# Optimization experiments

Measured on AMD Instinct MI355X. Metric: run time of the kernel, lower is better.

The kernel has to match this reference:

```python
import jax, jax.numpy as jnp
import numpy as np

D_MODEL = 1024
N_HEADS = 16
SEQ = 2048
BATCH = 2
EPS = 1e-5


def layer_norm(x, g, b):
    mu = jnp.mean(x, axis=-1, keepdims=True)
    var = jnp.mean(jnp.square(x - mu), axis=-1, keepdims=True)
    return (x - mu) * jax.lax.rsqrt(var + EPS) * g + b


def setup_inputs() -> dict:
    key = jax.random.key(0)
    ks = jax.random.split(key, 10)
    D = D_MODEL
    s = lambda fan_in: 1.0 / np.sqrt(fan_in)
    return {
        "x": jax.random.normal(ks[0], (BATCH, SEQ, D), dtype=jnp.float32),
        # weights stored [in, out] (torch Linear is y = x @ W.T; equivalent math)
        "w_attn": jax.random.uniform(ks[1], (D, 3 * D), minval=-s(D), maxval=s(D), dtype=jnp.float32),
        "b_attn": jnp.zeros((3 * D,), jnp.float32),
        "w_proj": jax.random.uniform(ks[2], (D, D), minval=-s(D), maxval=s(D), dtype=jnp.float32),
        "b_proj": jnp.zeros((D,), jnp.float32),
        "ln1_g": jnp.ones((D,), jnp.float32),
        "ln1_b": jnp.zeros((D,), jnp.float32),
        "ln2_g": jnp.ones((D,), jnp.float32),
        "ln2_b": jnp.zeros((D,), jnp.float32),
        "w_fc1": jax.random.uniform(ks[3], (D, 4 * D), minval=-s(D), maxval=s(D), dtype=jnp.float32),
        "b_fc1": jnp.zeros((4 * D,), jnp.float32),
        "w_fc2": jax.random.uniform(ks[4], (4 * D, D), minval=-s(4 * D), maxval=s(4 * D), dtype=jnp.float32),
        "b_fc2": jnp.zeros((D,), jnp.float32),
    }


def reference(x, w_attn, b_attn, w_proj, b_proj, ln1_g, ln1_b, ln2_g, ln2_b, w_fc1, b_fc1, w_fc2, b_fc2):
    B, L, D = x.shape
    H = N_HEADS
    Dh = D // H

    # --- attention sublayer ---
    h = layer_norm(x, ln1_g, ln1_b)
    qkv = h @ w_attn + b_attn                      # [B, L, 3D]
    # SOURCE BUG (faithful): q, k, v are all taken from the k third.
    k = qkv[..., D:2 * D]
    kh = k.reshape(B, L, H, Dh).transpose(0, 2, 1, 3)   # [B, H, L, Dh]
    att = jnp.einsum('bhqd,bhkd->bhqk', kh, kh) / jnp.sqrt(jnp.float32(Dh))
    att = jax.nn.softmax(att, axis=-1)
    out = jnp.einsum('bhqk,bhkd->bhqd', att, kh)         # [B, H, L, Dh]
    out = out.transpose(0, 2, 1, 3).reshape(B, L, D)
    x = x + (out @ w_proj + b_proj)

    # --- feed-forward sublayer ---
    h = layer_norm(x, ln2_g, ln2_b)
    h = jax.nn.relu(h @ w_fc1 + b_fc1)
    x = x + (h @ w_fc2 + b_fc2)
    return x
```

## Files before the change

### kernel.cpp

```cpp
#include <hip/hip_runtime.h>


typedef __attribute__((ext_vector_type(8))) short s8v;
typedef __attribute__((ext_vector_type(4))) float f4v;

#define D_MODEL 1024
#define SEQ 2048
#define BATCH 2
#define NH 16
#define DH 64
#define MROWS (BATCH * SEQ)

__device__ __forceinline__ float b2f(unsigned short u) {
  union { unsigned int i; float f; } v; v.i = ((unsigned int)u) << 16; return v.f;
}
__device__ __forceinline__ unsigned short f2b(float f) {
  unsigned int i = __builtin_bit_cast(unsigned int, f);
  unsigned int r = (i + 0x7fffu + ((i >> 16) & 1u)) >> 16;
  return (unsigned short)r;
}
__device__ __forceinline__ void async16(const void* g, void* l) {
  __builtin_amdgcn_global_load_lds(
      (const __attribute__((address_space(1))) unsigned int*)g,
      (__attribute__((address_space(3))) unsigned int*)l, 16, 0, 0);
}
__device__ __forceinline__ unsigned short cvt_b(float f) { return f2b(f); }
__device__ __forceinline__ unsigned short cvt_b(unsigned short u) { return u; }

__global__ __launch_bounds__(256) void ln_kernel(
    const float* __restrict__ x, const float* __restrict__ g,
    const float* __restrict__ bb, unsigned short* __restrict__ out) {
  int row = blockIdx.x;
  int t = threadIdx.x;
  const float* xr = x + (size_t)row * D_MODEL;
  float v[4];
  float s = 0.f, s2 = 0.f;
#pragma unroll
  for (int i = 0; i < 4; ++i) {
    float f = xr[t + 256 * i];
    v[i] = f; s += f; s2 += f * f;
  }
#pragma unroll
  for (int off = 1; off < 64; off <<= 1) {
    s += __shfl_xor(s, off, 64);
    s2 += __shfl_xor(s2, off, 64);
  }
  __shared__ float red[8];
  if ((t & 63) == 0) { red[t >> 6] = s; red[4 + (t >> 6)] = s2; }
  __syncthreads();
  s = red[0] + red[1] + red[2] + red[3];
  s2 = red[4] + red[5] + red[6] + red[7];
  float mu = s * (1.f / D_MODEL);
  float var = s2 * (1.f / D_MODEL) - mu * mu;
  float rstd = rsqrtf(var + 1e-5f);
#pragma unroll
  for (int i = 0; i < 4; ++i) {
    int c = t + 256 * i;
    float h = (v[i] - mu) * rstd * g[c] + bb[c];
    out[(size_t)row * D_MODEL + c] = f2b(h);
  }
}

template <typename T>
__global__ __launch_bounds__(256) void transpose_b(
    const T* __restrict__ src, unsigned short* __restrict__ dst,
    int srcStride, int dstStride, long long srcBatch, long long dstBatch) {
  __shared__ unsigned short tile[64][65];
  const T* s = src + (size_t)blockIdx.z * srcBatch;
  unsigned short* d = dst + (size_t)blockIdx.z * dstBatch;
  int n0 = blockIdx.x * 64, k0 = blockIdx.y * 64;
  for (int i = threadIdx.x; i < 4096; i += 256) {
    int k = i >> 6, n = i & 63;
    tile[k][n] = cvt_b(s[(size_t)(k0 + k) * srcStride + n0 + n]);
  }
  __syncthreads();
  for (int i = threadIdx.x; i < 4096; i += 256) {
    int n = i >> 6, k = i & 63;
    d[(size_t)(n0 + n) * dstStride + k0 + k] = tile[k][n];
  }
}

template <int RES, bool RELU, bool KH, int OUTF, int BN>
__global__ __launch_bounds__(256) void gemm_bt(
    const unsigned short* __restrict__ A, const unsigned short* __restrict__ Bt,
    const float* __restrict__ bias, const float* __restrict__ res,
    void* __restrict__ out, int M, int N, int K) {
  constexpr int NT = BN / 32;
  __shared__ __align__(16) unsigned short lsA[128 * 64];
  __shared__ __align__(16) unsigned short lsB[BN * 64];
  int tid = threadIdx.x;
  int lane = tid & 63, w = tid >> 6, quad = lane >> 4, l16 = lane & 15;
  int m0 = blockIdx.y * 128, n0 = blockIdx.x * BN;
  int wm = (w >> 1) * 64, wn = (w & 1) * (BN / 2);
  f4v acc[4][NT] = {};
  for (int kt = 0; kt < K; kt += 64) {
#pragma unroll
    for (int i = 0; i < 4; ++i) {
      int cb = w * 256 + i * 64;
      int ci = cb + lane;
      int row = ci >> 3, c = ci & 7;
      int cs = c ^ (row & 7);
      async16(A + (size_t)(m0 + row) * K + kt + cs * 8, &lsA[cb * 8]);
    }
#pragma unroll
    for (int i = 0; i < BN / 32; ++i) {
      int cb = w * (BN * 2) + i * 64;
      int ci = cb + lane;
      int row = ci >> 3, c = ci & 7;
      int cs = c ^ (row & 7);
      async16(Bt + (size_t)(n0 + row) * K + kt + cs * 8, &lsB[cb * 8]);
    }
    __builtin_amdgcn_s_waitcnt(0x0f70);
    __syncthreads();
#pragma unroll
    for (int s = 0; s < 2; ++s) {
      s8v af[4], bf[NT];
#pragma unroll
      for (int t = 0; t < 4; ++t) {
        int am = wm + t * 16 + l16;
        int ac = (s * 4 + quad) ^ (am & 7);
        af[t] = *(const s8v*)(&lsA[am * 64 + ac * 8]);
      }
#pragma unroll
      for (int t = 0; t < NT; ++t) {
        int bn = wn + t * 16 + l16;
        int bc = (s * 4 + quad) ^ (bn & 7);
        bf[t] = *(const s8v*)(&lsB[bn * 64 + bc * 8]);
      }
#pragma unroll
      for (int ti = 0; ti < 4; ++ti)
#pragma unroll
        for (int tj = 0; tj < NT; ++tj)
          acc[ti][tj] = __builtin_amdgcn_mfma_f32_16x16x32_bf16(
              af[ti], bf[tj], acc[ti][tj], 0, 0, 0);
    }
    __syncthreads();
  }
#pragma unroll
  for (int tj = 0; tj < NT; ++tj) {
    int col = n0 + wn + tj * 16 + l16;
    float bv = bias[col];
#pragma unroll
    for (int ti = 0; ti < 4; ++ti) {
#pragma unroll
      for (int r = 0; r < 4; ++r) {
        int rowg = m0 + wm + ti * 16 + quad * 4 + r;
        float vv = acc[ti][tj][r] + bv;
        if (RES == 2) vv += res[(size_t)rowg * N + col];
        if (RELU) vv = fmaxf(vv, 0.f);
        size_t oidx;
        if (KH) {
          int b = rowg >> 11, l = rowg & 2047, h = col >> 6, d = col & 63;
          oidx = (((size_t)(b * NH + h)) * SEQ + l) * DH + d;
        } else {
          oidx = (size_t)rowg * N + col;
        }
        if (OUTF == 0) ((unsigned short*)out)[oidx] = f2b(vv);
        else           ((float*)out)[oidx] = vv;
      }
    }
  }
}

__global__ __launch_bounds__(256) void flash_k(
    const unsigned short* __restrict__ kh, const unsigned short* __restrict__ khT,
    float* __restrict__ Opart, float* __restrict__ lpart) {
  __shared__ __align__(16) unsigned short lsK[64 * 64];
  __shared__ __align__(16) unsigned short lsKT[64 * 64];
  __shared__ __align__(16) unsigned short lsP[4][32 * 72];
  int tid = threadIdx.x;
  int lane = tid & 63, w = tid >> 6, quad = lane >> 4, l16 = lane & 15;
  int qb = blockIdx.x, bh = blockIdx.y, split = blockIdx.z;
  const unsigned short* khB = kh + (size_t)bh * SEQ * DH;
  const unsigned short* khTB = khT + (size_t)bh * DH * SEQ;
  float* Op = Opart + (size_t)split * MROWS * D_MODEL;
  float* lp = lpart + (size_t)split * BATCH * NH * SEQ;
  s8v aQ[2][2];
#pragma unroll
  for (int g = 0; g < 2; ++g) {
    int q = qb * 128 + w * 32 + g * 16 + l16;
#pragma unroll
    for (int s = 0; s < 2; ++s)
      aQ[g][s] = *(const s8v*)(khB + (size_t)q * DH + s * 32 + quad * 8);
  }
  float l_part[2][4] = {};
  f4v accO[2][4] = {};
  const float kexp = 0.18033688f;

  for (int kt = split * 16; kt < split * 16 + 16; ++kt) {
#pragma unroll
    for (int i = 0; i < 2; ++i) {
      int cb = w * 128 + i * 64;
      int ci = cb + lane;
      int row = ci >> 3, c = ci & 7;
      int cs = c ^ (row & 7);
      async16(khB + (size_t)(kt * 64 + row) * DH + cs * 8, &lsK[cb * 8]);
      async16(khTB + (size_t)row * SEQ + kt * 64 + cs * 8, &lsKT[cb * 8]);
    }
    __builtin_amdgcn_s_waitcnt(0x0f70);
    __syncthreads();
    f4v accS[2][4] = {};
#pragma unroll
    for (int s = 0; s < 2; ++s) {
#pragma unroll
      for (int tj = 0; tj < 4; ++tj) {
        int key = tj * 16 + l16;
        int c = (s * 4 + quad) ^ (key & 7);
        s8v bK = *(const s8v*)(&lsK[key * 64 + c * 8]);
#pragma unroll
        for (int g = 0; g < 2; ++g)
          accS[g][tj] = __builtin_amdgcn_mfma_f32_16x16x32_bf16(
              aQ[g][s], bK, accS[g][tj], 0, 0, 0);
      }
    }
    unsigned short* Pb = lsP[w];
#pragma unroll
    for (int g = 0; g < 2; ++g)
#pragma unroll
      for (int tj = 0; tj < 4; ++tj)
#pragma unroll
        for (int r = 0; r < 4; ++r) {
          float p = exp2f(accS[g][tj][r] * kexp);
          l_part[g][r] += p;
          unsigned int pb = __builtin_bit_cast(unsigned int, p * 1.00195312f);
          Pb[(g * 16 + quad * 4 + r) * 72 + tj * 16 + l16] =
              (unsigned short)(pb >> 16);
        }
#pragma unroll
    for (int s2 = 0; s2 < 2; ++s2) {
      s8v aP[2];
#pragma unroll
      for (int g = 0; g < 2; ++g)
        aP[g] = *(const s8v*)(&Pb[(g * 16 + l16) * 72 + s2 * 32 + quad * 8]);
#pragma unroll
      for (int db = 0; db < 4; ++db) {
        int d = db * 16 + l16;
        int c = (s2 * 4 + quad) ^ (d & 7);
        s8v bV = *(const s8v*)(&lsKT[d * 64 + c * 8]);
#pragma unroll
        for (int g = 0; g < 2; ++g)
          accO[g][db] = __builtin_amdgcn_mfma_f32_16x16x32_bf16(
              aP[g], bV, accO[g][db], 0, 0, 0);
      }
    }
    __syncthreads();
  }
  int b = bh >> 4, h = bh & 15;
#pragma unroll
  for (int g = 0; g < 2; ++g)
#pragma unroll
    for (int r = 0; r < 4; ++r) {
      float lpv = l_part[g][r];
#pragma unroll
      for (int off = 1; off < 16; off <<= 1) lpv += __shfl_xor(lpv, off, 64);
      int l = qb * 128 + w * 32 + g * 16 + quad * 4 + r;
      if (l16 == 0) lp[(size_t)bh * SEQ + l] = lpv;
#pragma unroll
      for (int db = 0; db < 4; ++db) {
        int d = db * 16 + l16;
        Op[((size_t)(b * SEQ + l)) * D_MODEL + h * DH + d] = accO[g][db][r];
      }
    }
}

__global__ __launch_bounds__(256) void attn_combine(
    const float* __restrict__ Opart, const float* __restrict__ lpart,
    unsigned short* __restrict__ attn) {
  int row = blockIdx.x;
  int b = row >> 11, l = row & 2047;
  int c0 = threadIdx.x * 4;
  int h = c0 >> 6;
  size_t lidx = (size_t)(b * NH + h) * SEQ + l;
  float ls = lpart[lidx] + lpart[(size_t)BATCH * NH * SEQ + lidx];
  float inv = 1.f / ls;
  const float4 o0 = *(const float4*)(Opart + (size_t)row * D_MODEL + c0);
  const float4 o1 = *(const float4*)(Opart + (size_t)MROWS * D_MODEL +
                                     (size_t)row * D_MODEL + c0);
  unsigned short* op = attn + (size_t)row * D_MODEL + c0;
  op[0] = f2b((o0.x + o1.x) * inv);
  op[1] = f2b((o0.y + o1.y) * inv);
  op[2] = f2b((o0.z + o1.z) * inv);
  op[3] = f2b((o0.w + o1.w) * inv);
}

extern "C" void kernel_launch(void* const* d_in, const int* in_sizes, int n_in,
                              void* d_out, int out_size, void* d_ws, size_t ws_size,
                              hipStream_t stream) {
  (void)in_sizes; (void)n_in; (void)out_size;
  const float* x      = (const float*)d_in[0];
  const float* w_attn = (const float*)d_in[1];
  const float* b_attn = (const float*)d_in[2];
  const float* w_proj = (const float*)d_in[3];
  const float* b_proj = (const float*)d_in[4];
  const float* ln1_g  = (const float*)d_in[5];
  const float* ln1_b  = (const float*)d_in[6];
  const float* ln2_g  = (const float*)d_in[7];
  const float* ln2_b  = (const float*)d_in[8];
  const float* w_fc1  = (const float*)d_in[9];
  const float* b_fc1  = (const float*)d_in[10];
  const float* w_fc2  = (const float*)d_in[11];
  const float* b_fc2  = (const float*)d_in[12];

  char* ws = (char*)d_ws;
  float*          x1    = (float*)(ws);
  unsigned short* hbuf  = (unsigned short*)(ws + (size_t)(16u << 20));
  unsigned short* wT1   = (unsigned short*)(ws + (size_t)(24u << 20));
  unsigned short* wT2   = (unsigned short*)(ws + (size_t)(32u << 20));
  unsigned short* kh    = (unsigned short*)(ws + (size_t)(40u << 20));
  unsigned short* khT   = (unsigned short*)(ws + (size_t)(48u << 20));
  float*          Opart = (float*)(ws);
  float*          lpart = (float*)(ws + (size_t)(32u << 20));
  unsigned short* fc1o  = kh;
  unsigned short* attn  = (unsigned short*)d_out;
  float* outf = (float*)d_out;
  bool big_ws = ws_size >= ((size_t)72u << 20);

  dim3 blk(256);
  hipLaunchKernelGGL(ln_kernel, dim3(MROWS), blk, 0, stream, x, ln1_g, ln1_b, hbuf);
  hipLaunchKernelGGL(transpose_b<float>, dim3(16, 16, 1), blk, 0, stream,
                     w_attn + 1024, wT1, 3 * D_MODEL, D_MODEL, 0LL, 0LL);
  hipLaunchKernelGGL((gemm_bt<0, false, true, 0, 64>), dim3(16, 32), blk, 0, stream,
                     hbuf, wT1, b_attn + 1024, nullptr, (void*)kh,
                     MROWS, D_MODEL, D_MODEL);
  hipLaunchKernelGGL(transpose_b<unsigned short>, dim3(1, 32, 32), blk, 0, stream,
                     kh, khT, DH, SEQ, (long long)(SEQ * DH), (long long)(DH * SEQ));
  hipLaunchKernelGGL(flash_k, dim3(SEQ / 128, BATCH * NH, 2), blk, 0, stream,
                     kh, khT, Opart, lpart);
  hipLaunchKernelGGL(attn_combine, dim3(MROWS), blk, 0, stream,
                     Opart, lpart, attn);
  hipLaunchKernelGGL(transpose_b<float>, dim3(16, 16, 1), blk, 0, stream,
                     w_proj, wT1, D_MODEL, D_MODEL, 0LL, 0LL);
  hipLaunchKernelGGL((gemm_bt<2, false, false, 1, 64>), dim3(16, 32), blk, 0, stream,
                     attn, wT1, b_proj, x, (void*)x1, MROWS, D_MODEL, D_MODEL);
  hipLaunchKernelGGL(ln_kernel, dim3(MROWS), blk, 0, stream, x1, ln2_g, ln2_b, hbuf);
  hipLaunchKernelGGL(transpose_b<float>, dim3(64, 16, 1), blk, 0, stream,
                     w_fc1, wT1, 4 * D_MODEL, D_MODEL, 0LL, 0LL);
  hipLaunchKernelGGL(transpose_b<float>, dim3(16, 64, 1), blk, 0, stream,
                     w_fc2, wT2, D_MODEL, 4 * D_MODEL, 0LL, 0LL);
  if (big_ws) {
    hipLaunchKernelGGL((gemm_bt<0, true, false, 0, 128>), dim3(32, 32), blk, 0, stream,
                       hbuf, wT1, b_fc1, nullptr, (void*)fc1o,
                       MROWS, 4 * D_MODEL, D_MODEL);
    hipLaunchKernelGGL((gemm_bt<2, false, false, 1, 64>), dim3(16, 32), blk, 0, stream,
                       fc1o, wT2, b_fc2, x1, (void*)outf,
                       MROWS, D_MODEL, 4 * D_MODEL);
  } else {
    for (int c = 0; c < 2; ++c) {
      const unsigned short* h2c = hbuf + (size_t)c * 2048 * D_MODEL;
      const float* x1c = x1 + (size_t)c * 2048 * D_MODEL;
      float* outc = outf + (size_t)c * 2048 * D_MODEL;
      hipLaunchKernelGGL((gemm_bt<0, true, false, 0, 128>), dim3(32, 16), blk, 0, stream,
                         h2c, wT1, b_fc1, nullptr, (void*)fc1o,
                         2048, 4 * D_MODEL, D_MODEL);
      hipLaunchKernelGGL((gemm_bt<2, false, false, 1, 64>), dim3(16, 16), blk, 0, stream,
                         fc1o, wT2, b_fc2, x1c, (void*)outc,
                         2048, D_MODEL, 4 * D_MODEL);
    }
  }
}
```

Baseline: 377.1 us.

## Keep attention probabilities in registers via transposed S and store bf16 partials

The score MFMA is computed transposed (K as A operand, Q as B) so each lane's accumulator already matches the layout of the A operand of a 16x16x16 bf16 MFMA. P can then feed the PV product straight from registers, which removes the per-wave LDS round trip for P. The split-K partial outputs are stored as bf16 instead of fp32, halving their write and read traffic in attn_combine. In exchange the PV MFMAs use a narrower K=16 instruction (twice as many issues), and the unnormalised partial sums lose precision when rounded to bf16.

```diff
diff --git a/kernel.cpp b/kernel.cpp
--- a/kernel.cpp
+++ b/kernel.cpp
@@ -2,6 +2,7 @@
 
 
 typedef __attribute__((ext_vector_type(8))) short s8v;
+typedef __attribute__((ext_vector_type(4))) short s4v;
 typedef __attribute__((ext_vector_type(4))) float f4v;
 
 #define D_MODEL 1024
@@ -26,6 +27,22 @@
 }
 __device__ __forceinline__ unsigned short cvt_b(float f) { return f2b(f); }
 __device__ __forceinline__ unsigned short cvt_b(unsigned short u) { return u; }
+
+#if __has_builtin(__builtin_amdgcn_mfma_f32_16x16x16_bf16)
+__device__ __forceinline__ f4v mfma16(s4v a, s4v b, f4v c) {
+  return __builtin_amdgcn_mfma_f32_16x16x16_bf16(a, b, c, 0, 0, 0);
+}
+#elif __has_builtin(__builtin_amdgcn_mfma_f32_16x16x16bf16_1k)
+__device__ __forceinline__ f4v mfma16(s4v a, s4v b, f4v c) {
+  return __builtin_amdgcn_mfma_f32_16x16x16bf16_1k(a, b, c, 0, 0, 0);
+}
+#else
+__device__ __forceinline__ f4v mfma16(s4v a, s4v b, f4v c) {
+  s8v aa = {a[0], a[1], a[2], a[3], 0, 0, 0, 0};
+  s8v bb = {b[0], b[1], b[2], b[3], 0, 0, 0, 0};
+  return __builtin_amdgcn_mfma_f32_16x16x32_bf16(aa, bb, c, 0, 0, 0);
+}
+#endif
 
 __global__ __launch_bounds__(256) void ln_kernel(
     const float* __restrict__ x, const float* __restrict__ g,
@@ -164,16 +181,15 @@
 
 __global__ __launch_bounds__(256) void flash_k(
     const unsigned short* __restrict__ kh, const unsigned short* __restrict__ khT,
-    float* __restrict__ Opart, float* __restrict__ lpart) {
+    unsigned short* __restrict__ Opart, float* __restrict__ lpart) {
   __shared__ __align__(16) unsigned short lsK[64 * 64];
   __shared__ __align__(16) unsigned short lsKT[64 * 64];
-  __shared__ __align__(16) unsigned short lsP[4][32 * 72];
   int tid = threadIdx.x;
   int lane = tid & 63, w = tid >> 6, quad = lane >> 4, l16 = lane & 15;
   int qb = blockIdx.x, bh = blockIdx.y, split = blockIdx.z;
   const unsigned short* khB = kh + (size_t)bh * SEQ * DH;
   const unsigned short* khTB = khT + (size_t)bh * DH * SEQ;
-  float* Op = Opart + (size_t)split * MROWS * D_MODEL;
+  unsigned short* Op = Opart + (size_t)split * MROWS * D_MODEL;
   float* lp = lpart + (size_t)split * BATCH * NH * SEQ;
   s8v aQ[2][2];
 #pragma unroll
@@ -183,7 +199,7 @@
     for (int s = 0; s < 2; ++s)
       aQ[g][s] = *(const s8v*)(khB + (size_t)q * DH + s * 32 + quad * 8);
   }
-  float l_part[2][4] = {};
+  float l_lane[2] = {0.f, 0.f};
   f4v accO[2][4] = {};
   const float kexp = 0.18033688f;
 
@@ -199,72 +215,69 @@
     }
     __builtin_amdgcn_s_waitcnt(0x0f70);
     __syncthreads();
-    f4v accS[2][4] = {};
+    f4v accST[2][4] = {};
 #pragma unroll
     for (int s = 0; s < 2; ++s) {
 #pragma unroll
       for (int tj = 0; tj < 4; ++tj) {
         int key = tj * 16 + l16;
         int c = (s * 4 + quad) ^ (key & 7);
-        s8v bK = *(const s8v*)(&lsK[key * 64 + c * 8]);
+        s8v kf = *(const s8v*)(&lsK[key * 64 + c * 8]);
 #pragma unroll
         for (int g = 0; g < 2; ++g)
-          accS[g][tj] = __builtin_amdgcn_mfma_f32_16x16x32_bf16(
-              aQ[g][s], bK, accS[g][tj], 0, 0, 0);
-      }
-    }
-    unsigned short* Pb = lsP[w];
-#pragma unroll
-    for (int g = 0; g < 2; ++g)
-#pragma unroll
-      for (int tj = 0; tj < 4; ++tj)
+          accST[g][tj] = __builtin_amdgcn_mfma_f32_16x16x32_bf16(
+              kf, aQ[g][s], accST[g][tj], 0, 0, 0);
+      }
+    }
+#pragma unroll
+    for (int tj = 0; tj < 4; ++tj) {
+      s4v pf[2];
+#pragma unroll
+      for (int g = 0; g < 2; ++g) {
 #pragma unroll
         for (int r = 0; r < 4; ++r) {
-          float p = exp2f(accS[g][tj][r] * kexp);
-          l_part[g][r] += p;
+          float p = exp2f(accST[g][tj][r] * kexp);
+          l_lane[g] += p;
           unsigned int pb = __builtin_bit_cast(unsigned int, p * 1.00195312f);
-          Pb[(g * 16 + quad * 4 + r) * 72 + tj * 16 + l16] =
-              (unsigned short)(pb >> 16);
+          pf[g][r] = (short)(pb >> 16);
         }
-#pragma unroll
-    for (int s2 = 0; s2 < 2; ++s2) {
-      s8v aP[2];
-#pragma unroll
-      for (int g = 0; g < 2; ++g)
-        aP[g] = *(const s8v*)(&Pb[(g * 16 + l16) * 72 + s2 * 32 + quad * 8]);
+      }
 #pragma unroll
       for (int db = 0; db < 4; ++db) {
         int d = db * 16 + l16;
-        int c = (s2 * 4 + quad) ^ (d & 7);
-        s8v bV = *(const s8v*)(&lsKT[d * 64 + c * 8]);
+        int ch = (tj * 2 + (quad >> 1)) ^ (d & 7);
+        s4v vf = *(const s4v*)(&lsKT[d * 64 + ch * 8 + (quad & 1) * 4]);
 #pragma unroll
         for (int g = 0; g < 2; ++g)
-          accO[g][db] = __builtin_amdgcn_mfma_f32_16x16x32_bf16(
-              aP[g], bV, accO[g][db], 0, 0, 0);
+          accO[g][db] = mfma16(pf[g], vf, accO[g][db]);
       }
     }
     __syncthreads();
   }
   int b = bh >> 4, h = bh & 15;
 #pragma unroll
-  for (int g = 0; g < 2; ++g)
+  for (int g = 0; g < 2; ++g) {
+    float lv = l_lane[g];
+    lv += __shfl_xor(lv, 16, 64);
+    lv += __shfl_xor(lv, 32, 64);
+    if (quad == 0) {
+      int q = qb * 128 + w * 32 + g * 16 + l16;
+      lp[(size_t)bh * SEQ + q] = lv;
+    }
 #pragma unroll
     for (int r = 0; r < 4; ++r) {
-      float lpv = l_part[g][r];
-#pragma unroll
-      for (int off = 1; off < 16; off <<= 1) lpv += __shfl_xor(lpv, off, 64);
       int l = qb * 128 + w * 32 + g * 16 + quad * 4 + r;
-      if (l16 == 0) lp[(size_t)bh * SEQ + l] = lpv;
 #pragma unroll
       for (int db = 0; db < 4; ++db) {
         int d = db * 16 + l16;
-        Op[((size_t)(b * SEQ + l)) * D_MODEL + h * DH + d] = accO[g][db][r];
-      }
-    }
+        Op[((size_t)(b * SEQ + l)) * D_MODEL + h * DH + d] = f2b(accO[g][db][r]);
+      }
+    }
+  }
 }
 
 __global__ __launch_bounds__(256) void attn_combine(
-    const float* __restrict__ Opart, const float* __restrict__ lpart,
+    const unsigned short* __restrict__ Opart, const float* __restrict__ lpart,
     unsigned short* __restrict__ attn) {
   int row = blockIdx.x;
   int b = row >> 11, l = row & 2047;
@@ -273,14 +286,15 @@
   size_t lidx = (size_t)(b * NH + h) * SEQ + l;
   float ls = lpart[lidx] + lpart[(size_t)BATCH * NH * SEQ + lidx];
   float inv = 1.f / ls;
-  const float4 o0 = *(const float4*)(Opart + (size_t)row * D_MODEL + c0);
-  const float4 o1 = *(const float4*)(Opart + (size_t)MROWS * D_MODEL +
-                                     (size_t)row * D_MODEL + c0);
-  unsigned short* op = attn + (size_t)row * D_MODEL + c0;
-  op[0] = f2b((o0.x + o1.x) * inv);
-  op[1] = f2b((o0.y + o1.y) * inv);
-  op[2] = f2b((o0.z + o1.z) * inv);
-  op[3] = f2b((o0.w + o1.w) * inv);
+  s4v o0 = *(const s4v*)(Opart + (size_t)row * D_MODEL + c0);
+  s4v o1 = *(const s4v*)(Opart + (size_t)MROWS * D_MODEL +
+                         (size_t)row * D_MODEL + c0);
+  s4v ov;
+#pragma unroll
+  for (int i = 0; i < 4; ++i)
+    ov[i] = (short)f2b((b2f((unsigned short)o0[i]) +
+                        b2f((unsigned short)o1[i])) * inv);
+  *(s4v*)(attn + (size_t)row * D_MODEL + c0) = ov;
 }
 
 extern "C" void kernel_launch(void* const* d_in, const int* in_sizes, int n_in,
@@ -308,8 +322,8 @@
   unsigned short* wT2   = (unsigned short*)(ws + (size_t)(32u << 20));
   unsigned short* kh    = (unsigned short*)(ws + (size_t)(40u << 20));
   unsigned short* khT   = (unsigned short*)(ws + (size_t)(48u << 20));
-  float*          Opart = (float*)(ws);
-  float*          lpart = (float*)(ws + (size_t)(32u << 20));
+  unsigned short* Opart = (unsigned short*)(ws);
+  float*          lpart = (float*)(ws + (size_t)(16u << 20));
   unsigned short* fc1o  = kh;
   unsigned short* attn  = (unsigned short*)d_out;
   float* outf = (float*)d_out;
```

Result: no change. 370.9 us (-1.6%).
